# Optimization experiments

Hardware: AMD Instinct MI355X
Metric: run time of the kernel (lower is better)

## Reference

```python
import jax, jax.numpy as jnp
import numpy as np

B, S, D, V, H, L = 2, 64, 1024, 32000, 8, 2
HD = D // H

def setup_inputs():
    key = jax.random.key(0)
    ks = jax.random.split(key, 12)
    w = lambda k, shp: jax.random.normal(k, shp, jnp.float32) * 0.02
    return {
        "embedded_answer": jax.random.normal(ks[0], (B, S, D), jnp.float32),
        "sa_in_w": w(ks[1], (L, 3 * D, D)), "sa_in_b": jnp.zeros((L, 3 * D), jnp.float32),
        "sa_out_w": w(ks[2], (L, D, D)), "sa_out_b": jnp.zeros((L, D), jnp.float32),
        "ca_in_w": w(ks[3], (L, 3 * D, D)), "ca_in_b": jnp.zeros((L, 3 * D), jnp.float32),
        "ca_out_w": w(ks[4], (L, D, D)), "ca_out_b": jnp.zeros((L, D), jnp.float32),
        "ff1_w": w(ks[5], (L, 4 * D, D)), "ff1_b": jnp.zeros((L, 4 * D), jnp.float32),
        "ff2_w": w(ks[6], (L, D, 4 * D)), "ff2_b": jnp.zeros((L, D), jnp.float32),
        "ln_w": jnp.ones((L, 3, D), jnp.float32), "ln_b": jnp.zeros((L, 3, D), jnp.float32),
        "out_w": w(ks[7], (V, D)), "out_b": jnp.zeros((V,), jnp.float32),
        "temp_w": w(ks[8], (1, D)), "temp_b": jnp.zeros((1,), jnp.float32),
        "len_w": w(ks[9], (1, D)), "len_b": jnp.zeros((1,), jnp.float32),
        "style_w": w(ks[10], (D, D)), "style_b": jnp.zeros((D,), jnp.float32),
        "num_steps": 8,
    }

def _ln(x, w, b, eps=1e-5):
    m = x.mean(-1, keepdims=True)
    v = ((x - m) ** 2).mean(-1, keepdims=True)
    return (x - m) * jax.lax.rsqrt(v + eps) * w + b

def _mha(q_in, kv_in, in_w, in_b, ow, ob):
    wq, wk, wv = jnp.split(in_w, 3, 0)
    bq, bk, bv = jnp.split(in_b, 3, 0)
    q = (q_in @ wq.T + bq).reshape(q_in.shape[0], q_in.shape[1], H, HD)
    k = (kv_in @ wk.T + bk).reshape(kv_in.shape[0], kv_in.shape[1], H, HD)
    v = (kv_in @ wv.T + bv).reshape(kv_in.shape[0], kv_in.shape[1], H, HD)
    a = jax.nn.softmax(jnp.einsum('bqhd,bkhd->bhqk', q, k) * (HD ** -0.5), axis=-1)
    o = jnp.einsum('bhqk,bkhd->bqhd', a, v).reshape(q_in.shape)
    return o @ ow.T + ob

def _decode(x, mem, l, p):
    # post-LN torch TransformerDecoderLayer (relu FFN, no masks, eval/no dropout)
    x = _ln(x + _mha(x, x, p['sa_in_w'][l], p['sa_in_b'][l], p['sa_out_w'][l], p['sa_out_b'][l]), p['ln_w'][l, 0], p['ln_b'][l, 0])
    x = _ln(x + _mha(x, mem, p['ca_in_w'][l], p['ca_in_b'][l], p['ca_out_w'][l], p['ca_out_b'][l]), p['ln_w'][l, 1], p['ln_b'][l, 1])
    h = jax.nn.relu(x @ p['ff1_w'][l].T + p['ff1_b'][l]) @ p['ff2_w'][l].T + p['ff2_b'][l]
    return _ln(x + h, p['ln_w'][l, 2], p['ln_b'][l, 2])

def reference(embedded_answer, sa_in_w, sa_in_b, sa_out_w, sa_out_b, ca_in_w, ca_in_b, ca_out_w, ca_out_b, ff1_w, ff1_b, ff2_w, ff2_b, ln_w, ln_b, out_w, out_b, temp_w, temp_b, len_w, len_b, style_w, style_b, num_steps):
    p = dict(sa_in_w=sa_in_w, sa_in_b=sa_in_b, sa_out_w=sa_out_w, sa_out_b=sa_out_b,
             ca_in_w=ca_in_w, ca_in_b=ca_in_b, ca_out_w=ca_out_w, ca_out_b=ca_out_b,
             ff1_w=ff1_w, ff1_b=ff1_b, ff2_w=ff2_w, ff2_b=ff2_b, ln_w=ln_w, ln_b=ln_b)
    # control_generation (per-batch mean temperature / mean style vector)
    temp = jax.nn.sigmoid(embedded_answer @ temp_w.T + temp_b).mean(axis=(1, 2))[:, None]  # [B,1]
    _length_factor = jax.nn.sigmoid(embedded_answer @ len_w.T + len_b)  # drives static num_steps
    style = (embedded_answer @ style_w.T + style_b).mean(axis=1, keepdims=True)  # [B,1,D]
    cur = embedded_answer
    skey = jax.random.key(42)
    toks, lgs = [], []
    for t in range(num_steps):  # static unrolled decode loop; full recompute (no KV cache), as original
        h = cur
        for l in range(L):
            h = _decode(h, embedded_answer, l, p)
        logits_last = ((h + style)[:, -1, :] @ out_w.T + out_b) / temp  # [B,V]
        nt = jax.random.categorical(jax.random.fold_in(skey, t), logits_last)  # == softmax+multinomial
        toks.append(nt)
        lgs.append(logits_last)
        cur = jnp.concatenate([cur, out_w[nt][:, None, :]], axis=1)  # re-embed via output weight rows
    return jnp.stack(toks, 1), jnp.stack(lgs, 1)
```

## Files before the change

### kernel.cpp

```cpp
#include <hip/hip_runtime.h>
#include <stdint.h>

__host__ __device__ inline void threefry2x32(uint32_t k0, uint32_t k1,
                                             uint32_t x0, uint32_t x1,
                                             uint32_t* o0, uint32_t* o1) {
  uint32_t ks2 = 0x1BD11BDAu ^ k0 ^ k1;
  x0 += k0; x1 += k1;
#define TF_R(x, r) (((x) << (r)) | ((x) >> (32 - (r))))
#define TF_ROUND(r) { x0 += x1; x1 = TF_R(x1, r); x1 ^= x0; }
  TF_ROUND(13) TF_ROUND(15) TF_ROUND(26) TF_ROUND(6)
  x0 += k1; x1 += ks2 + 1u;
  TF_ROUND(17) TF_ROUND(29) TF_ROUND(16) TF_ROUND(24)
  x0 += ks2; x1 += k0 + 2u;
  TF_ROUND(13) TF_ROUND(15) TF_ROUND(26) TF_ROUND(6)
  x0 += k0; x1 += k1 + 3u;
  TF_ROUND(17) TF_ROUND(29) TF_ROUND(16) TF_ROUND(24)
  x0 += k1; x1 += ks2 + 4u;
  TF_ROUND(13) TF_ROUND(15) TF_ROUND(26) TF_ROUND(6)
  x0 += ks2; x1 += k0 + 5u;
  *o0 = x0; *o1 = x1;
#undef TF_ROUND
#undef TF_R
}

__device__ __forceinline__ float wave_sum(float v) {
#pragma unroll
  for (int o = 32; o > 0; o >>= 1) v += __shfl_xor(v, o, 64);
  return v;
}
__device__ __forceinline__ float wave_max(float v) {
#pragma unroll
  for (int o = 32; o > 0; o >>= 1) v = fmaxf(v, __shfl_xor(v, o, 64));
  return v;
}

__global__ __launch_bounds__(256) void gemm2_kernel(
    const float* __restrict__ X, long long xbs, int ldx,
    const float* __restrict__ W, int ldw,
    const float* __restrict__ bias,
    float* __restrict__ out, long long obs, int ldo,
    int St, int M, int N, int K32, int relu, int partial) {
  __shared__ __align__(16) float Xl[2][32][68];
  __shared__ __align__(16) float Wl[2][32][68];
  const int tid = threadIdx.x;
  const int m0 = blockIdx.x * 64;
  const int n0 = blockIdx.y * 64;
  const long long kbase = (long long)blockIdx.z * K32 * 32;
  const int mi = tid >> 4;
  const int ni = tid & 15;
  const int lr = tid >> 3;
  const int lc = (tid & 7) * 4;

  const int mA = m0 + lr, mB = m0 + lr + 32;
  const float* xpA = nullptr;
  const float* xpB = nullptr;
  if (mA < M) {
    int b = mA / St, s = mA - b * St;
    xpA = X + (long long)b * xbs + (long long)s * ldx + kbase + lc;
  }
  if (mB < M) {
    int b = mB / St, s = mB - b * St;
    xpB = X + (long long)b * xbs + (long long)s * ldx + kbase + lc;
  }
  const float* wpA = W + (long long)(n0 + lr) * ldw + kbase + lc;
  const float* wpB = W + (long long)(n0 + lr + 32) * ldw + kbase + lc;

  float4 xA = xpA ? *(const float4*)xpA : make_float4(0.f, 0.f, 0.f, 0.f);
  float4 xB = xpB ? *(const float4*)xpB : make_float4(0.f, 0.f, 0.f, 0.f);
  float4 wA = *(const float4*)wpA;
  float4 wB = *(const float4*)wpB;

  float acc[4][4];
#pragma unroll
  for (int i = 0; i < 4; ++i)
#pragma unroll
    for (int j = 0; j < 4; ++j) acc[i][j] = 0.f;

  Xl[0][lc + 0][lr] = xA.x; Xl[0][lc + 1][lr] = xA.y;
  Xl[0][lc + 2][lr] = xA.z; Xl[0][lc + 3][lr] = xA.w;
  Xl[0][lc + 0][lr + 32] = xB.x; Xl[0][lc + 1][lr + 32] = xB.y;
  Xl[0][lc + 2][lr + 32] = xB.z; Xl[0][lc + 3][lr + 32] = xB.w;
  Wl[0][lc + 0][lr] = wA.x; Wl[0][lc + 1][lr] = wA.y;
  Wl[0][lc + 2][lr] = wA.z; Wl[0][lc + 3][lr] = wA.w;
  Wl[0][lc + 0][lr + 32] = wB.x; Wl[0][lc + 1][lr + 32] = wB.y;
  Wl[0][lc + 2][lr + 32] = wB.z; Wl[0][lc + 3][lr + 32] = wB.w;
  __syncthreads();

  for (int i = 0; i < K32; ++i) {
    if (i + 1 < K32) {
      int off = (i + 1) * 32;
      xA = xpA ? *(const float4*)(xpA + off) : make_float4(0.f, 0.f, 0.f, 0.f);
      xB = xpB ? *(const float4*)(xpB + off) : make_float4(0.f, 0.f, 0.f, 0.f);
      wA = *(const float4*)(wpA + off);
      wB = *(const float4*)(wpB + off);
    }
    const int cur = i & 1;
#pragma unroll
    for (int kk = 0; kk < 32; ++kk) {
      float4 xv = *(const float4*)&Xl[cur][kk][mi * 4];
      float4 wv = *(const float4*)&Wl[cur][kk][ni * 4];
      float xa[4] = {xv.x, xv.y, xv.z, xv.w};
      float wa[4] = {wv.x, wv.y, wv.z, wv.w};
#pragma unroll
      for (int a = 0; a < 4; ++a)
#pragma unroll
        for (int c = 0; c < 4; ++c) acc[a][c] = fmaf(xa[a], wa[c], acc[a][c]);
    }
    if (i + 1 < K32) {
      __syncthreads();
      const int nxt = cur ^ 1;
      Xl[nxt][lc + 0][lr] = xA.x; Xl[nxt][lc + 1][lr] = xA.y;
      Xl[nxt][lc + 2][lr] = xA.z; Xl[nxt][lc + 3][lr] = xA.w;
      Xl[nxt][lc + 0][lr + 32] = xB.x; Xl[nxt][lc + 1][lr + 32] = xB.y;
      Xl[nxt][lc + 2][lr + 32] = xB.z; Xl[nxt][lc + 3][lr + 32] = xB.w;
      Wl[nxt][lc + 0][lr] = wA.x; Wl[nxt][lc + 1][lr] = wA.y;
      Wl[nxt][lc + 2][lr] = wA.z; Wl[nxt][lc + 3][lr] = wA.w;
      Wl[nxt][lc + 0][lr + 32] = wB.x; Wl[nxt][lc + 1][lr + 32] = wB.y;
      Wl[nxt][lc + 2][lr + 32] = wB.z; Wl[nxt][lc + 3][lr + 32] = wB.w;
      __syncthreads();
    }
  }

  const int n = n0 + ni * 4;
  if (partial) {
    float* base = out + (long long)blockIdx.z * M * ldo;
#pragma unroll
    for (int i = 0; i < 4; ++i) {
      int m = m0 + mi * 4 + i;
      if (m >= M) continue;
      *(float4*)(base + (long long)m * ldo + n) =
          make_float4(acc[i][0], acc[i][1], acc[i][2], acc[i][3]);
    }
  } else {
    float4 bv = *(const float4*)(bias + n);
#pragma unroll
    for (int i = 0; i < 4; ++i) {
      int m = m0 + mi * 4 + i;
      if (m >= M) continue;
      int b = m / St, s = m - b * St;
      float4 o;
      o.x = acc[i][0] + bv.x; o.y = acc[i][1] + bv.y;
      o.z = acc[i][2] + bv.z; o.w = acc[i][3] + bv.w;
      if (relu) {
        o.x = fmaxf(o.x, 0.f); o.y = fmaxf(o.y, 0.f);
        o.z = fmaxf(o.z, 0.f); o.w = fmaxf(o.w, 0.f);
      }
      *(float4*)(out + (long long)b * obs + (long long)s * ldo + n) = o;
    }
  }
}

__global__ __launch_bounds__(256) void epi_kernel(
    const float* __restrict__ P, int splits, int M, int N,
    const float* __restrict__ bias,
    const float* __restrict__ res, long long rbs, int ldr,
    const float* __restrict__ lnw, const float* __restrict__ lnb,
    float* __restrict__ out, long long obs, int ldo, int St, int relu) {
  __shared__ float red[4];
  const int m = blockIdx.x;
  const int b = m / St, s = m - b * St;
  const int n = blockIdx.y * 1024 + threadIdx.x * 4;
  const float* pr = P + (long long)m * N + n;
  float4 v = *(const float4*)pr;
  for (int sp = 1; sp < splits; ++sp) {
    float4 w2 = *(const float4*)(pr + (long long)sp * M * N);
    v.x += w2.x; v.y += w2.y; v.z += w2.z; v.w += w2.w;
  }
  float4 bv = *(const float4*)(bias + n);
  v.x += bv.x; v.y += bv.y; v.z += bv.z; v.w += bv.w;
  if (res) {
    float4 rv = *(const float4*)(res + (long long)b * rbs + (long long)s * ldr + n);
    v.x += rv.x; v.y += rv.y; v.z += rv.z; v.w += rv.w;
  }
  if (relu) {
    v.x = fmaxf(v.x, 0.f); v.y = fmaxf(v.y, 0.f);
    v.z = fmaxf(v.z, 0.f); v.w = fmaxf(v.w, 0.f);
  }
  if (lnw) {
    const int tid = threadIdx.x;
    float sum = wave_sum(v.x + v.y + v.z + v.w);
    int wid = tid >> 6;
    if ((tid & 63) == 0) red[wid] = sum;
    __syncthreads();
    float mean = (red[0] + red[1] + red[2] + red[3]) * (1.f / 1024.f);
    float4 d;
    d.x = v.x - mean; d.y = v.y - mean; d.z = v.z - mean; d.w = v.w - mean;
    float s2 = wave_sum(d.x * d.x + d.y * d.y + d.z * d.z + d.w * d.w);
    __syncthreads();
    if ((tid & 63) == 0) red[wid] = s2;
    __syncthreads();
    float var = (red[0] + red[1] + red[2] + red[3]) * (1.f / 1024.f);
    float inv = rsqrtf(var + 1e-5f);
    float4 wv = *(const float4*)(lnw + tid * 4);
    float4 lb = *(const float4*)(lnb + tid * 4);
    v.x = d.x * inv * wv.x + lb.x;
    v.y = d.y * inv * wv.y + lb.y;
    v.z = d.z * inv * wv.z + lb.z;
    v.w = d.w * inv * wv.w + lb.w;
  }
  *(float4*)(out + (long long)b * obs + (long long)s * ldo + n) = v;
}

__global__ __launch_bounds__(64) void attn_kernel(
    const float* __restrict__ Qp, int q_rs, long long q_bs,
    const float* __restrict__ Qp2,
    const float* __restrict__ qbias,
    const float* __restrict__ Kp, int k_rs, long long k_bs,
    const float* __restrict__ Vp, int v_rs, long long v_bs,
    float* __restrict__ Op, int o_rs, long long o_bs,
    int Sq, int Skv) {
  const int lane = threadIdx.x;
  int bid = blockIdx.x;
  int b = bid / (8 * Sq);
  int rr = bid - b * 8 * Sq;
  int h = rr / Sq;
  int sq = rr - h * Sq;
  const float* qrow = Qp + (long long)b * q_bs + (long long)sq * q_rs + h * 128;
  float q0 = qrow[lane], q1 = qrow[lane + 64];
  if (Qp2) {
    const float* q2 = Qp2 + (long long)b * q_bs + (long long)sq * q_rs + h * 128;
    q0 += q2[lane]; q1 += q2[lane + 64];
  }
  if (qbias) {
    q0 += qbias[h * 128 + lane]; q1 += qbias[h * 128 + lane + 64];
  }
  __shared__ float sc[72];
  const float* kb = Kp + (long long)b * k_bs + h * 128;
  for (int sk = 0; sk < Skv; ++sk) {
    const float* kr = kb + (long long)sk * k_rs;
    float p = fmaf(q0, kr[lane], q1 * kr[lane + 64]);
    p = wave_sum(p);
    if (lane == 0) sc[sk] = p * 0.08838834764831845f;
  }
  __syncthreads();
  float m = -3.4e38f;
  for (int i = lane; i < Skv; i += 64) m = fmaxf(m, sc[i]);
  m = wave_max(m);
  float ssum = 0.f;
  for (int i = lane; i < Skv; i += 64) {
    float e = expf(sc[i] - m);
    sc[i] = e;
    ssum += e;
  }
  ssum = wave_sum(ssum);
  __syncthreads();
  float o0 = 0.f, o1 = 0.f;
  const float* vb = Vp + (long long)b * v_bs + h * 128;
  for (int sk = 0; sk < Skv; ++sk) {
    float w = sc[sk];
    const float* vr = vb + (long long)sk * v_rs;
    o0 = fmaf(w, vr[lane], o0);
    o1 = fmaf(w, vr[lane + 64], o1);
  }
  float inv = 1.f / ssum;
  float* orow = Op + (long long)b * o_bs + (long long)sq * o_rs + h * 128;
  orow[lane] = o0 * inv;
  orow[lane + 64] = o1 * inv;
}

__global__ __launch_bounds__(256) void copy_cur_kernel(
    const float* __restrict__ emb, float* __restrict__ cur) {
  int idx = blockIdx.x * 256 + threadIdx.x;
  int b = idx >> 16;
  int r = idx & 65535;
  cur[(long long)b * 73728 + r] = emb[idx];
}

__global__ __launch_bounds__(256) void xmean_kernel(
    const float* __restrict__ emb, float* __restrict__ xmean) {
  int idx = blockIdx.x * 256 + threadIdx.x;
  int b = idx >> 10, d = idx & 1023;
  float s = 0.f;
  for (int ss = 0; ss < 64; ++ss) s += emb[b * 65536 + ss * 1024 + d];
  xmean[idx] = s * (1.f / 64.f);
}

__global__ __launch_bounds__(256) void temp_kernel(
    const float* __restrict__ emb, const float* __restrict__ tw,
    const float* __restrict__ tb, float* __restrict__ tempv) {
  __shared__ float red[4];
  int b = blockIdx.x;
  int wid = threadIdx.x >> 6, lane = threadIdx.x & 63;
  float acc = 0.f;
  for (int s = wid; s < 64; s += 4) {
    const float* x = emb + b * 65536 + s * 1024;
    float p = 0.f;
#pragma unroll
    for (int it = 0; it < 4; ++it) {
      float4 xv = *(const float4*)(x + it * 256 + lane * 4);
      float4 wv = *(const float4*)(tw + it * 256 + lane * 4);
      p += xv.x * wv.x + xv.y * wv.y + xv.z * wv.z + xv.w * wv.w;
    }
    p = wave_sum(p);
    acc += 1.f / (1.f + expf(-(p + tb[0])));
  }
  if (lane == 0) red[wid] = acc;
  __syncthreads();
  if (threadIdx.x == 0)
    tempv[b] = (red[0] + red[1] + red[2] + red[3]) * (1.f / 64.f);
}

__global__ __launch_bounds__(256) void style_kernel(
    const float* __restrict__ xmean, const float* __restrict__ sw,
    const float* __restrict__ sb, float* __restrict__ stylev) {
  int wid = threadIdx.x >> 6, lane = threadIdx.x & 63;
  int d = blockIdx.x * 4 + wid;
  const float* wr = sw + (long long)d * 1024;
  float a0 = 0.f, a1 = 0.f;
#pragma unroll
  for (int it = 0; it < 4; ++it) {
    float4 wv = *(const float4*)(wr + it * 256 + lane * 4);
    float4 x0 = *(const float4*)(xmean + it * 256 + lane * 4);
    float4 x1 = *(const float4*)(xmean + 1024 + it * 256 + lane * 4);
    a0 += wv.x * x0.x + wv.y * x0.y + wv.z * x0.z + wv.w * x0.w;
    a1 += wv.x * x1.x + wv.y * x1.y + wv.z * x1.z + wv.w * x1.w;
  }
  a0 = wave_sum(a0);
  a1 = wave_sum(a1);
  if (lane == 0) {
    stylev[d] = a0 + sb[d];
    stylev[1024 + d] = a1 + sb[d];
  }
}

__global__ __launch_bounds__(256) void logits_kernel(
    const float* __restrict__ A, const float* __restrict__ stylev, int St,
    const float* __restrict__ Wo, const float* __restrict__ bo,
    const float* __restrict__ tempv, float* __restrict__ outl, int t) {
  int wid = threadIdx.x >> 6, lane = threadIdx.x & 63;
  int n = blockIdx.x * 4 + wid;
  const float* wr = Wo + (long long)n * 1024;
  const float* a0p = A + (long long)(St - 1) * 1024;
  const float* a1p = A + 73728 + (long long)(St - 1) * 1024;
  float a0 = 0.f, a1 = 0.f;
#pragma unroll
  for (int it = 0; it < 4; ++it) {
    int off = it * 256 + lane * 4;
    float4 wv = *(const float4*)(wr + off);
    float4 x0 = *(const float4*)(a0p + off);
    float4 s0 = *(const float4*)(stylev + off);
    float4 x1 = *(const float4*)(a1p + off);
    float4 s1 = *(const float4*)(stylev + 1024 + off);
    float4 z0 = make_float4(x0.x + s0.x, x0.y + s0.y, x0.z + s0.z, x0.w + s0.w);
    float4 z1 = make_float4(x1.x + s1.x, x1.y + s1.y, x1.z + s1.z, x1.w + s1.w);
    a0 += wv.x * z0.x + wv.y * z0.y + wv.z * z0.z + wv.w * z0.w;
    a1 += wv.x * z1.x + wv.y * z1.y + wv.z * z1.z + wv.w * z1.w;
  }
  a0 = wave_sum(a0);
  a1 = wave_sum(a1);
  if (lane == 0) {
    float bb = bo[n];
    outl[(long long)(0 * 8 + t) * 32000 + n] = (a0 + bb) / tempv[0];
    outl[(long long)(1 * 8 + t) * 32000 + n] = (a1 + bb) / tempv[1];
  }
}

__global__ __launch_bounds__(1024) void sample_kernel(
    const float* __restrict__ logits, const float* __restrict__ Wo,
    float* __restrict__ tok_f, float* __restrict__ cur, int St,
    uint32_t fk0, uint32_t fk1, int t) {
  int b = blockIdx.x;
  const float* lg = logits + (long long)(b * 8 + t) * 32000;
  float best = -3.4e38f;
  int bi = 0x7fffffff;
  for (int n = threadIdx.x; n < 32000; n += 1024) {
    uint32_t r0, r1;
    threefry2x32(fk0, fk1, 0u, (uint32_t)(b * 32000 + n), &r0, &r1);
    uint32_t bits = (r0 ^ r1) >> 9;
    float u = __uint_as_float(0x3f800000u | bits) - 1.0f;
    if (u < 1.1754944e-38f) u = 1.1754944e-38f;
    float g = -logf(-logf(u));
    float val = lg[n] + g;
    if (val > best) { best = val; bi = n; }
  }
  __shared__ float bv[1024];
  __shared__ int bix[1024];
  bv[threadIdx.x] = best;
  bix[threadIdx.x] = bi;
  __syncthreads();
  for (int s = 512; s > 0; s >>= 1) {
    if (threadIdx.x < s) {
      float ov = bv[threadIdx.x + s];
      int oi = bix[threadIdx.x + s];
      if (ov > bv[threadIdx.x] ||
          (ov == bv[threadIdx.x] && oi < bix[threadIdx.x])) {
        bv[threadIdx.x] = ov;
        bix[threadIdx.x] = oi;
      }
    }
    __syncthreads();
  }
  int tok = bix[0];
  if (threadIdx.x == 0) tok_f[b * 8 + t] = (float)tok;
  cur[(long long)b * 73728 + (long long)St * 1024 + threadIdx.x] =
      Wo[(long long)tok * 1024 + threadIdx.x];
}

static inline void g2(hipStream_t st, const float* X, long long xbs, int ldx,
                      const float* W, int ldw, const float* bias, float* out,
                      long long obs, int ldo, int St, int M, int N, int K,
                      int splits, int relu, int partial) {
  dim3 grid((unsigned)((M + 63) / 64), (unsigned)(N / 64), (unsigned)splits);
  gemm2_kernel<<<grid, 256, 0, st>>>(X, xbs, ldx, W, ldw, bias, out, obs, ldo,
                                     St, M, N, K / (32 * splits), relu,
                                     partial);
}

static inline void epi(hipStream_t st, const float* P, int splits, int M,
                       int N, const float* bias, const float* res,
                       long long rbs, int ldr, const float* lnw,
                       const float* lnb, float* out, long long obs, int ldo,
                       int St, int relu) {
  dim3 grid((unsigned)M, (unsigned)(N / 1024));
  epi_kernel<<<grid, 256, 0, st>>>(P, splits, M, N, bias, res, rbs, ldr, lnw,
                                   lnb, out, obs, ldo, St, relu);
}

extern "C" void kernel_launch(void* const* d_in, const int* in_sizes, int n_in,
                              void* d_out, int out_size, void* d_ws,
                              size_t ws_size, hipStream_t stream) {
  const float* emb = (const float*)d_in[0];
  const float* sa_in_w = (const float*)d_in[1];
  const float* sa_in_b = (const float*)d_in[2];
  const float* sa_out_w = (const float*)d_in[3];
  const float* sa_out_b = (const float*)d_in[4];
  const float* ca_in_w = (const float*)d_in[5];
  const float* ca_in_b = (const float*)d_in[6];
  const float* ca_out_w = (const float*)d_in[7];
  const float* ca_out_b = (const float*)d_in[8];
  const float* ff1_w = (const float*)d_in[9];
  const float* ff1_b = (const float*)d_in[10];
  const float* ff2_w = (const float*)d_in[11];
  const float* ff2_b = (const float*)d_in[12];
  const float* ln_w = (const float*)d_in[13];
  const float* ln_b = (const float*)d_in[14];
  const float* out_w = (const float*)d_in[15];
  const float* out_b = (const float*)d_in[16];
  const float* temp_w = (const float*)d_in[17];
  const float* temp_b = (const float*)d_in[18];
  const float* style_w = (const float*)d_in[21];
  const float* style_b = (const float*)d_in[22];

  float* ws = (float*)d_ws;
  float* cur = ws;
  float* A = cur + 2 * 72 * 1024;
  float* Qb = A + 2 * 72 * 1024;
  float* Tb = Qb + 2 * 72 * 3072;
  float* Fb = Tb + 2 * 72 * 1024;
  float* cakv = Fb + 2 * 72 * 4096;
  float* Pp = cakv + 2 * 2 * 64 * 2048;
  float* xmean = Pp + 1310720;
  float* stylev = xmean + 2048;
  float* tempv = stylev + 2048;

  float* toks_out = (float*)d_out;
  float* logits_out = toks_out + 16;

  copy_cur_kernel<<<512, 256, 0, stream>>>(emb, cur);
  xmean_kernel<<<8, 256, 0, stream>>>(emb, xmean);
  temp_kernel<<<2, 256, 0, stream>>>(emb, temp_w, temp_b, tempv);
  style_kernel<<<256, 256, 0, stream>>>(xmean, style_w, style_b, stylev);
  for (int l = 0; l < 2; ++l) {
    g2(stream, emb, 64 * 1024, 1024,
       ca_in_w + (size_t)(l * 3072 + 1024) * 1024, 1024,
       ca_in_b + l * 3072 + 1024, cakv + (size_t)l * 2 * 64 * 2048, 64 * 2048,
       2048, 64, 128, 2048, 1024, 1, 0, 0);
  }

  for (int t = 0; t < 8; ++t) {
    int St = 64 + t;
    int M = 2 * St;
    for (int l = 0; l < 2; ++l) {
      const float* P0 = (l == 0) ? cur : A;
      g2(stream, P0, 72 * 1024, 1024, sa_in_w + (size_t)l * 3072 * 1024, 1024,
         sa_in_b + l * 3072, Qb, 72 * 3072, 3072, St, M, 3072, 1024, 1, 0, 0);
      attn_kernel<<<2 * 8 * St, 64, 0, stream>>>(
          Qb, 3072, 72 * 3072, nullptr, nullptr, Qb + 1024, 3072, 72 * 3072,
          Qb + 2048, 3072, 72 * 3072, Tb, 1024, 72 * 1024, St, St);
      g2(stream, Tb, 72 * 1024, 1024, sa_out_w + (size_t)l * 1024 * 1024, 1024,
         nullptr, Pp, 0, 1024, St, M, 1024, 1024, 4, 0, 1);
      epi(stream, Pp, 4, M, 1024, sa_out_b + l * 1024, P0, 72 * 1024, 1024,
          ln_w + (l * 3 + 0) * 1024, ln_b + (l * 3 + 0) * 1024, A, 72 * 1024,
          1024, St, 0);
      g2(stream, A, 72 * 1024, 1024, ca_in_w + (size_t)l * 3072 * 1024, 1024,
         nullptr, Pp, 0, 1024, St, M, 1024, 1024, 2, 0, 1);
      attn_kernel<<<2 * 8 * St, 64, 0, stream>>>(
          Pp, 1024, (long long)St * 1024, Pp + (size_t)M * 1024,
          ca_in_b + l * 3072, cakv + (size_t)l * 2 * 64 * 2048, 2048,
          64 * 2048, cakv + (size_t)l * 2 * 64 * 2048 + 1024, 2048, 64 * 2048,
          Tb, 1024, 72 * 1024, St, 64);
      g2(stream, Tb, 72 * 1024, 1024, ca_out_w + (size_t)l * 1024 * 1024, 1024,
         nullptr, Pp, 0, 1024, St, M, 1024, 1024, 4, 0, 1);
      epi(stream, Pp, 4, M, 1024, ca_out_b + l * 1024, A, 72 * 1024, 1024,
          ln_w + (l * 3 + 1) * 1024, ln_b + (l * 3 + 1) * 1024, A, 72 * 1024,
          1024, St, 0);
      g2(stream, A, 72 * 1024, 1024, ff1_w + (size_t)l * 4096 * 1024, 1024,
         ff1_b + l * 4096, Fb, 72 * 4096, 4096, St, M, 4096, 1024, 1, 1, 0);
      g2(stream, Fb, 72 * 4096, 4096, ff2_w + (size_t)l * 1024 * 4096, 4096,
         nullptr, Pp, 0, 1024, St, M, 1024, 4096, 8, 0, 1);
      epi(stream, Pp, 8, M, 1024, ff2_b + l * 1024, A, 72 * 1024, 1024,
          ln_w + (l * 3 + 2) * 1024, ln_b + (l * 3 + 2) * 1024, A, 72 * 1024,
          1024, St, 0);
    }
    logits_kernel<<<8000, 256, 0, stream>>>(A, stylev, St, out_w, out_b,
                                            tempv, logits_out, t);
    uint32_t fk0, fk1;
    threefry2x32(0u, 42u, 0u, (uint32_t)t, &fk0, &fk1);
    sample_kernel<<<2, 1024, 0, stream>>>(logits_out, out_w, toks_out, cur,
                                          St, fk0, fk1, t);
  }
}
```

Measured before the change: 5.834 ms.

## Fuse split-K reduction, residual and LayerNorm into GEMM via last-block atomics

Replaces the separate GEMM plus epilogue kernels with one GEMM that writes split-K partials and lets the last arriving block per tile, found with an atomic counter, reduce them and add bias, residual and ReLU. A second counter per row lets the last tile compute LayerNorm statistics. The normalization is then applied lazily when the next GEMM, the residual path or the logits kernel loads the data. Split counts go up for most GEMMs to raise parallelism. This removes the epilogue launches and their extra passes over memory, at the cost of threadfences, atomics, more partial-buffer traffic and recomputing the normalization on every load.

```diff
diff --git a/kernel.cpp b/kernel.cpp
--- a/kernel.cpp
+++ b/kernel.cpp
@@ -34,47 +34,73 @@
   return v;
 }
 
-__global__ __launch_bounds__(256) void gemm2_kernel(
+__global__ __launch_bounds__(256) void gemm3_kernel(
     const float* __restrict__ X, long long xbs, int ldx,
-    const float* __restrict__ W, int ldw,
-    const float* __restrict__ bias,
-    float* __restrict__ out, long long obs, int ldo,
-    int St, int M, int N, int K32, int relu, int partial) {
+    const float* __restrict__ xstats, const float* __restrict__ xlnw,
+    const float* __restrict__ xlnb,
+    const float* __restrict__ W, int ldw, const float* __restrict__ bias,
+    const float* __restrict__ resY, long long rbs, int ldr,
+    const float* __restrict__ rstats, const float* __restrict__ rlnw,
+    const float* __restrict__ rlnb,
+    float* __restrict__ Pp, float* __restrict__ out, long long obs, int ldo,
+    float* __restrict__ ostats,
+    int St, int M, int N, int K32, int relu,
+    int* __restrict__ tilecnt, int* __restrict__ rowcnt) {
   __shared__ __align__(16) float Xl[2][32][68];
   __shared__ __align__(16) float Wl[2][32][68];
+  __shared__ int sflag;
   const int tid = threadIdx.x;
   const int m0 = blockIdx.x * 64;
   const int n0 = blockIdx.y * 64;
+  const int splits = gridDim.z;
+  const int Nt = gridDim.y;
   const long long kbase = (long long)blockIdx.z * K32 * 32;
-  const int mi = tid >> 4;
-  const int ni = tid & 15;
-  const int lr = tid >> 3;
-  const int lc = (tid & 7) * 4;
+  const int mi = tid >> 4, ni = tid & 15, lr = tid >> 3, lc = (tid & 7) * 4;
+  const int wid = tid >> 6, lane = tid & 63;
 
   const int mA = m0 + lr, mB = m0 + lr + 32;
   const float* xpA = nullptr;
   const float* xpB = nullptr;
+  float mnA = 0.f, rsA = 1.f, mnB = 0.f, rsB = 1.f;
   if (mA < M) {
     int b = mA / St, s = mA - b * St;
     xpA = X + (long long)b * xbs + (long long)s * ldx + kbase + lc;
+    if (xstats) { mnA = xstats[2 * mA]; rsA = xstats[2 * mA + 1]; }
   }
   if (mB < M) {
     int b = mB / St, s = mB - b * St;
     xpB = X + (long long)b * xbs + (long long)s * ldx + kbase + lc;
+    if (xstats) { mnB = xstats[2 * mB]; rsB = xstats[2 * mB + 1]; }
   }
   const float* wpA = W + (long long)(n0 + lr) * ldw + kbase + lc;
   const float* wpB = W + (long long)(n0 + lr + 32) * ldw + kbase + lc;
+  const float* lwp = xlnw ? xlnw + kbase + lc : nullptr;
+  const float* lbp = xlnb ? xlnb + kbase + lc : nullptr;
 
   float4 xA = xpA ? *(const float4*)xpA : make_float4(0.f, 0.f, 0.f, 0.f);
   float4 xB = xpB ? *(const float4*)xpB : make_float4(0.f, 0.f, 0.f, 0.f);
   float4 wA = *(const float4*)wpA;
   float4 wB = *(const float4*)wpB;
+  float4 lw4 = make_float4(1.f, 1.f, 1.f, 1.f);
+  float4 lb4 = make_float4(0.f, 0.f, 0.f, 0.f);
+  if (lwp) { lw4 = *(const float4*)lwp; lb4 = *(const float4*)lbp; }
 
   float acc[4][4];
 #pragma unroll
   for (int i = 0; i < 4; ++i)
 #pragma unroll
     for (int j = 0; j < 4; ++j) acc[i][j] = 0.f;
+
+  if (xstats) {
+    xA.x = (xA.x - mnA) * rsA * lw4.x + lb4.x;
+    xA.y = (xA.y - mnA) * rsA * lw4.y + lb4.y;
+    xA.z = (xA.z - mnA) * rsA * lw4.z + lb4.z;
+    xA.w = (xA.w - mnA) * rsA * lw4.w + lb4.w;
+    xB.x = (xB.x - mnB) * rsB * lw4.x + lb4.x;
+    xB.y = (xB.y - mnB) * rsB * lw4.y + lb4.y;
+    xB.z = (xB.z - mnB) * rsB * lw4.z + lb4.z;
+    xB.w = (xB.w - mnB) * rsB * lw4.w + lb4.w;
+  }
 
   Xl[0][lc + 0][lr] = xA.x; Xl[0][lc + 1][lr] = xA.y;
   Xl[0][lc + 2][lr] = xA.z; Xl[0][lc + 3][lr] = xA.w;
@@ -93,6 +119,10 @@
       xB = xpB ? *(const float4*)(xpB + off) : make_float4(0.f, 0.f, 0.f, 0.f);
       wA = *(const float4*)(wpA + off);
       wB = *(const float4*)(wpB + off);
+      if (lwp) {
+        lw4 = *(const float4*)(lwp + off);
+        lb4 = *(const float4*)(lbp + off);
+      }
     }
     const int cur = i & 1;
 #pragma unroll
@@ -102,11 +132,22 @@
       float xa[4] = {xv.x, xv.y, xv.z, xv.w};
       float wa[4] = {wv.x, wv.y, wv.z, wv.w};
 #pragma unroll
-      for (int a = 0; a < 4; ++a)
-#pragma unroll
-        for (int c = 0; c < 4; ++c) acc[a][c] = fmaf(xa[a], wa[c], acc[a][c]);
+      for (int a2 = 0; a2 < 4; ++a2)
+#pragma unroll
+        for (int c2 = 0; c2 < 4; ++c2)
+          acc[a2][c2] = fmaf(xa[a2], wa[c2], acc[a2][c2]);
     }
     if (i + 1 < K32) {
+      if (xstats) {
+        xA.x = (xA.x - mnA) * rsA * lw4.x + lb4.x;
+        xA.y = (xA.y - mnA) * rsA * lw4.y + lb4.y;
+        xA.z = (xA.z - mnA) * rsA * lw4.z + lb4.z;
+        xA.w = (xA.w - mnA) * rsA * lw4.w + lb4.w;
+        xB.x = (xB.x - mnB) * rsB * lw4.x + lb4.x;
+        xB.y = (xB.y - mnB) * rsB * lw4.y + lb4.y;
+        xB.z = (xB.z - mnB) * rsB * lw4.z + lb4.z;
+        xB.w = (xB.w - mnB) * rsB * lw4.w + lb4.w;
+      }
       __syncthreads();
       const int nxt = cur ^ 1;
       Xl[nxt][lc + 0][lr] = xA.x; Xl[nxt][lc + 1][lr] = xA.y;
@@ -122,89 +163,97 @@
   }
 
   const int n = n0 + ni * 4;
-  if (partial) {
-    float* base = out + (long long)blockIdx.z * M * ldo;
+  {
+    float* base = Pp + (long long)blockIdx.z * M * N;
 #pragma unroll
     for (int i = 0; i < 4; ++i) {
       int m = m0 + mi * 4 + i;
       if (m >= M) continue;
-      *(float4*)(base + (long long)m * ldo + n) =
+      *(float4*)(base + (long long)m * N + n) =
           make_float4(acc[i][0], acc[i][1], acc[i][2], acc[i][3]);
     }
-  } else {
-    float4 bv = *(const float4*)(bias + n);
-#pragma unroll
-    for (int i = 0; i < 4; ++i) {
-      int m = m0 + mi * 4 + i;
+  }
+  __threadfence();
+  __syncthreads();
+  if (tid == 0)
+    sflag = (atomicAdd(tilecnt + blockIdx.y * gridDim.x + blockIdx.x, 1) ==
+             splits - 1);
+  __syncthreads();
+  if (!sflag) return;
+  __threadfence();
+
+  float4 bv = *(const float4*)(bias + n);
+#pragma unroll
+  for (int i = 0; i < 4; ++i) {
+    int m = m0 + mi * 4 + i;
+    if (m >= M) continue;
+    float4 v = make_float4(0.f, 0.f, 0.f, 0.f);
+    for (int sp = 0; sp < splits; ++sp) {
+      float4 p = *(const float4*)(Pp + (long long)sp * M * N +
+                                  (long long)m * N + n);
+      v.x += p.x; v.y += p.y; v.z += p.z; v.w += p.w;
+    }
+    v.x += bv.x; v.y += bv.y; v.z += bv.z; v.w += bv.w;
+    int b = m / St, s = m - b * St;
+    if (resY) {
+      float4 rv =
+          *(const float4*)(resY + (long long)b * rbs + (long long)s * ldr + n);
+      if (rstats) {
+        float rm = rstats[2 * m], rr = rstats[2 * m + 1];
+        float4 rw = *(const float4*)(rlnw + n);
+        float4 rb2 = *(const float4*)(rlnb + n);
+        rv.x = (rv.x - rm) * rr * rw.x + rb2.x;
+        rv.y = (rv.y - rm) * rr * rw.y + rb2.y;
+        rv.z = (rv.z - rm) * rr * rw.z + rb2.z;
+        rv.w = (rv.w - rm) * rr * rw.w + rb2.w;
+      }
+      v.x += rv.x; v.y += rv.y; v.z += rv.z; v.w += rv.w;
+    }
+    if (relu) {
+      v.x = fmaxf(v.x, 0.f); v.y = fmaxf(v.y, 0.f);
+      v.z = fmaxf(v.z, 0.f); v.w = fmaxf(v.w, 0.f);
+    }
+    *(float4*)(out + (long long)b * obs + (long long)s * ldo + n) = v;
+  }
+
+  if (ostats) {
+    __threadfence();
+    __syncthreads();
+    if (tid == 0)
+      sflag = (atomicAdd(rowcnt + blockIdx.x, 1) == Nt - 1);
+    __syncthreads();
+    if (!sflag) return;
+    __threadfence();
+    for (int r = wid; r < 64; r += 4) {
+      int m = m0 + r;
       if (m >= M) continue;
       int b = m / St, s = m - b * St;
-      float4 o;
-      o.x = acc[i][0] + bv.x; o.y = acc[i][1] + bv.y;
-      o.z = acc[i][2] + bv.z; o.w = acc[i][3] + bv.w;
-      if (relu) {
-        o.x = fmaxf(o.x, 0.f); o.y = fmaxf(o.y, 0.f);
-        o.z = fmaxf(o.z, 0.f); o.w = fmaxf(o.w, 0.f);
-      }
-      *(float4*)(out + (long long)b * obs + (long long)s * ldo + n) = o;
-    }
-  }
-}
-
-__global__ __launch_bounds__(256) void epi_kernel(
-    const float* __restrict__ P, int splits, int M, int N,
-    const float* __restrict__ bias,
-    const float* __restrict__ res, long long rbs, int ldr,
-    const float* __restrict__ lnw, const float* __restrict__ lnb,
-    float* __restrict__ out, long long obs, int ldo, int St, int relu) {
-  __shared__ float red[4];
-  const int m = blockIdx.x;
-  const int b = m / St, s = m - b * St;
-  const int n = blockIdx.y * 1024 + threadIdx.x * 4;
-  const float* pr = P + (long long)m * N + n;
-  float4 v = *(const float4*)pr;
-  for (int sp = 1; sp < splits; ++sp) {
-    float4 w2 = *(const float4*)(pr + (long long)sp * M * N);
-    v.x += w2.x; v.y += w2.y; v.z += w2.z; v.w += w2.w;
-  }
-  float4 bv = *(const float4*)(bias + n);
-  v.x += bv.x; v.y += bv.y; v.z += bv.z; v.w += bv.w;
-  if (res) {
-    float4 rv = *(const float4*)(res + (long long)b * rbs + (long long)s * ldr + n);
-    v.x += rv.x; v.y += rv.y; v.z += rv.z; v.w += rv.w;
-  }
-  if (relu) {
-    v.x = fmaxf(v.x, 0.f); v.y = fmaxf(v.y, 0.f);
-    v.z = fmaxf(v.z, 0.f); v.w = fmaxf(v.w, 0.f);
-  }
-  if (lnw) {
-    const int tid = threadIdx.x;
-    float sum = wave_sum(v.x + v.y + v.z + v.w);
-    int wid = tid >> 6;
-    if ((tid & 63) == 0) red[wid] = sum;
-    __syncthreads();
-    float mean = (red[0] + red[1] + red[2] + red[3]) * (1.f / 1024.f);
-    float4 d;
-    d.x = v.x - mean; d.y = v.y - mean; d.z = v.z - mean; d.w = v.w - mean;
-    float s2 = wave_sum(d.x * d.x + d.y * d.y + d.z * d.z + d.w * d.w);
-    __syncthreads();
-    if ((tid & 63) == 0) red[wid] = s2;
-    __syncthreads();
-    float var = (red[0] + red[1] + red[2] + red[3]) * (1.f / 1024.f);
-    float inv = rsqrtf(var + 1e-5f);
-    float4 wv = *(const float4*)(lnw + tid * 4);
-    float4 lb = *(const float4*)(lnb + tid * 4);
-    v.x = d.x * inv * wv.x + lb.x;
-    v.y = d.y * inv * wv.y + lb.y;
-    v.z = d.z * inv * wv.z + lb.z;
-    v.w = d.w * inv * wv.w + lb.w;
-  }
-  *(float4*)(out + (long long)b * obs + (long long)s * ldo + n) = v;
+      const float* row = out + (long long)b * obs + (long long)s * ldo;
+      float sm = 0.f;
+#pragma unroll
+      for (int it = 0; it < 4; ++it) {
+        float4 xv = *(const float4*)(row + it * 256 + lane * 4);
+        sm += xv.x + xv.y + xv.z + xv.w;
+      }
+      sm = wave_sum(sm) * (1.f / 1024.f);
+      float s2 = 0.f;
+#pragma unroll
+      for (int it = 0; it < 4; ++it) {
+        float4 xv = *(const float4*)(row + it * 256 + lane * 4);
+        float dx = xv.x - sm, dy = xv.y - sm, dz = xv.z - sm, dw = xv.w - sm;
+        s2 += dx * dx + dy * dy + dz * dz + dw * dw;
+      }
+      s2 = wave_sum(s2) * (1.f / 1024.f);
+      if (lane == 0) {
+        ostats[2 * m] = sm;
+        ostats[2 * m + 1] = rsqrtf(s2 + 1e-5f);
+      }
+    }
+  }
 }
 
 __global__ __launch_bounds__(64) void attn_kernel(
     const float* __restrict__ Qp, int q_rs, long long q_bs,
-    const float* __restrict__ Qp2,
-    const float* __restrict__ qbias,
     const float* __restrict__ Kp, int k_rs, long long k_bs,
     const float* __restrict__ Vp, int v_rs, long long v_bs,
     float* __restrict__ Op, int o_rs, long long o_bs,
@@ -217,13 +266,6 @@
   int sq = rr - h * Sq;
   const float* qrow = Qp + (long long)b * q_bs + (long long)sq * q_rs + h * 128;
   float q0 = qrow[lane], q1 = qrow[lane + 64];
-  if (Qp2) {
-    const float* q2 = Qp2 + (long long)b * q_bs + (long long)sq * q_rs + h * 128;
-    q0 += q2[lane]; q1 += q2[lane + 64];
-  }
-  if (qbias) {
-    q0 += qbias[h * 128 + lane]; q1 += qbias[h * 128 + lane + 64];
-  }
   __shared__ float sc[72];
   const float* kb = Kp + (long long)b * k_bs + h * 128;
   for (int sk = 0; sk < Skv; ++sk) {
@@ -324,27 +366,40 @@
 }
 
 __global__ __launch_bounds__(256) void logits_kernel(
-    const float* __restrict__ A, const float* __restrict__ stylev, int St,
-    const float* __restrict__ Wo, const float* __restrict__ bo,
-    const float* __restrict__ tempv, float* __restrict__ outl, int t) {
+    const float* __restrict__ Y, const float* __restrict__ ystats,
+    const float* __restrict__ lnw, const float* __restrict__ lnb, int St,
+    const float* __restrict__ stylev, const float* __restrict__ Wo,
+    const float* __restrict__ bo, const float* __restrict__ tempv,
+    float* __restrict__ outl, int t) {
   int wid = threadIdx.x >> 6, lane = threadIdx.x & 63;
   int n = blockIdx.x * 4 + wid;
   const float* wr = Wo + (long long)n * 1024;
-  const float* a0p = A + (long long)(St - 1) * 1024;
-  const float* a1p = A + 73728 + (long long)(St - 1) * 1024;
+  int m0 = St - 1, m1 = St + St - 1;
+  const float* y0 = Y + (long long)(St - 1) * 1024;
+  const float* y1 = Y + 73728 + (long long)(St - 1) * 1024;
+  float mean0 = ystats[2 * m0], rstd0 = ystats[2 * m0 + 1];
+  float mean1 = ystats[2 * m1], rstd1 = ystats[2 * m1 + 1];
   float a0 = 0.f, a1 = 0.f;
 #pragma unroll
   for (int it = 0; it < 4; ++it) {
     int off = it * 256 + lane * 4;
     float4 wv = *(const float4*)(wr + off);
-    float4 x0 = *(const float4*)(a0p + off);
+    float4 lw = *(const float4*)(lnw + off);
+    float4 lb = *(const float4*)(lnb + off);
     float4 s0 = *(const float4*)(stylev + off);
-    float4 x1 = *(const float4*)(a1p + off);
     float4 s1 = *(const float4*)(stylev + 1024 + off);
-    float4 z0 = make_float4(x0.x + s0.x, x0.y + s0.y, x0.z + s0.z, x0.w + s0.w);
-    float4 z1 = make_float4(x1.x + s1.x, x1.y + s1.y, x1.z + s1.z, x1.w + s1.w);
-    a0 += wv.x * z0.x + wv.y * z0.y + wv.z * z0.z + wv.w * z0.w;
-    a1 += wv.x * z1.x + wv.y * z1.y + wv.z * z1.z + wv.w * z1.w;
+    float4 x0 = *(const float4*)(y0 + off);
+    float4 x1 = *(const float4*)(y1 + off);
+    float z0x = (x0.x - mean0) * rstd0 * lw.x + lb.x + s0.x;
+    float z0y = (x0.y - mean0) * rstd0 * lw.y + lb.y + s0.y;
+    float z0z = (x0.z - mean0) * rstd0 * lw.z + lb.z + s0.z;
+    float z0w = (x0.w - mean0) * rstd0 * lw.w + lb.w + s0.w;
+    float z1x = (x1.x - mean1) * rstd1 * lw.x + lb.x + s1.x;
+    float z1y = (x1.y - mean1) * rstd1 * lw.y + lb.y + s1.y;
+    float z1z = (x1.z - mean1) * rstd1 * lw.z + lb.z + s1.z;
+    float z1w = (x1.w - mean1) * rstd1 * lw.w + lb.w + s1.w;
+    a0 += wv.x * z0x + wv.y * z0y + wv.z * z0z + wv.w * z0w;
+    a1 += wv.x * z1x + wv.y * z1y + wv.z * z1z + wv.w * z1w;
   }
   a0 = wave_sum(a0);
   a1 = wave_sum(a1);
@@ -394,26 +449,6 @@
   if (threadIdx.x == 0) tok_f[b * 8 + t] = (float)tok;
   cur[(long long)b * 73728 + (long long)St * 1024 + threadIdx.x] =
       Wo[(long long)tok * 1024 + threadIdx.x];
-}
-
-static inline void g2(hipStream_t st, const float* X, long long xbs, int ldx,
-                      const float* W, int ldw, const float* bias, float* out,
-                      long long obs, int ldo, int St, int M, int N, int K,
-                      int splits, int relu, int partial) {
-  dim3 grid((unsigned)((M + 63) / 64), (unsigned)(N / 64), (unsigned)splits);
-  gemm2_kernel<<<grid, 256, 0, st>>>(X, xbs, ldx, W, ldw, bias, out, obs, ldo,
-                                     St, M, N, K / (32 * splits), relu,
-                                     partial);
-}
-
-static inline void epi(hipStream_t st, const float* P, int splits, int M,
-                       int N, const float* bias, const float* res,
-                       long long rbs, int ldr, const float* lnw,
-                       const float* lnb, float* out, long long obs, int ldo,
-                       int St, int relu) {
-  dim3 grid((unsigned)M, (unsigned)(N / 1024));
-  epi_kernel<<<grid, 256, 0, st>>>(P, splits, M, N, bias, res, rbs, ldr, lnw,
-                                   lnb, out, obs, ldo, St, relu);
 }
 
 extern "C" void kernel_launch(void* const* d_in, const int* in_sizes, int n_in,
@@ -443,67 +478,102 @@
 
   float* ws = (float*)d_ws;
   float* cur = ws;
-  float* A = cur + 2 * 72 * 1024;
-  float* Qb = A + 2 * 72 * 1024;
-  float* Tb = Qb + 2 * 72 * 3072;
-  float* Fb = Tb + 2 * 72 * 1024;
-  float* cakv = Fb + 2 * 72 * 4096;
-  float* Pp = cakv + 2 * 2 * 64 * 2048;
-  float* xmean = Pp + 1310720;
+  float* Qb = cur + 147456;
+  float* Tb = Qb + 442368;
+  float* T2 = Tb + 147456;
+  float* Fb = T2 + 147456;
+  float* Yb = Fb + 589824;
+  float* cakv = Yb + 884736;
+  float* Pp = cakv + 524288;
+  float* xmean = Pp + 2400000;
   float* stylev = xmean + 2048;
   float* tempv = stylev + 2048;
+  float* statsb = tempv + 16;
+  int* cntpool = (int*)(statsb + 1728);
 
   float* toks_out = (float*)d_out;
   float* logits_out = toks_out + 16;
+
+  auto Y = [&](int l, int j) { return Yb + (size_t)(l * 3 + j) * 147456; };
+  auto SS = [&](int l, int j) { return statsb + (size_t)(l * 3 + j) * 288; };
+
+  hipMemsetAsync(cntpool, 0, 100 * 256 * sizeof(int), stream);
+
+  int inst = 0;
+  auto g3 = [&](const float* X, long long xbs, int ldx, const float* xst,
+                const float* xlw, const float* xlb, const float* W, int ldw,
+                const float* bias, const float* resY, long long rbs, int ldr,
+                const float* rst, const float* rlw, const float* rlb,
+                float* out, long long obs, int ldo, float* ost, int St, int M,
+                int N, int K, int splits, int relu) {
+    dim3 grid((unsigned)((M + 63) / 64), (unsigned)(N / 64),
+              (unsigned)splits);
+    int* tc = cntpool + inst * 256;
+    ++inst;
+    gemm3_kernel<<<grid, 256, 0, stream>>>(
+        X, xbs, ldx, xst, xlw, xlb, W, ldw, bias, resY, rbs, ldr, rst, rlw,
+        rlb, Pp, out, obs, ldo, ost, St, M, N, K / (32 * splits), relu, tc,
+        tc + 200);
+  };
 
   copy_cur_kernel<<<512, 256, 0, stream>>>(emb, cur);
   xmean_kernel<<<8, 256, 0, stream>>>(emb, xmean);
   temp_kernel<<<2, 256, 0, stream>>>(emb, temp_w, temp_b, tempv);
   style_kernel<<<256, 256, 0, stream>>>(xmean, style_w, style_b, stylev);
-  for (int l = 0; l < 2; ++l) {
-    g2(stream, emb, 64 * 1024, 1024,
+  for (int l = 0; l < 2; ++l)
+    g3(emb, 64 * 1024, 1024, nullptr, nullptr, nullptr,
        ca_in_w + (size_t)(l * 3072 + 1024) * 1024, 1024,
-       ca_in_b + l * 3072 + 1024, cakv + (size_t)l * 2 * 64 * 2048, 64 * 2048,
-       2048, 64, 128, 2048, 1024, 1, 0, 0);
-  }
+       ca_in_b + l * 3072 + 1024, nullptr, 0, 0, nullptr, nullptr, nullptr,
+       cakv + (size_t)l * 2 * 64 * 2048, 64 * 2048, 2048, nullptr, 64, 128,
+       2048, 1024, 4, 0);
 
   for (int t = 0; t < 8; ++t) {
-    int St = 64 + t;
-    int M = 2 * St;
+    const int St = 64 + t;
+    const int M = 2 * St;
     for (int l = 0; l < 2; ++l) {
-      const float* P0 = (l == 0) ? cur : A;
-      g2(stream, P0, 72 * 1024, 1024, sa_in_w + (size_t)l * 3072 * 1024, 1024,
-         sa_in_b + l * 3072, Qb, 72 * 3072, 3072, St, M, 3072, 1024, 1, 0, 0);
+      const float* X0 = (l == 0) ? cur : Y(0, 2);
+      const float* X0st = (l == 0) ? nullptr : SS(0, 2);
+      const float* X0lw = (l == 0) ? nullptr : ln_w + (0 * 3 + 2) * 1024;
+      const float* X0lb = (l == 0) ? nullptr : ln_b + (0 * 3 + 2) * 1024;
+
+      g3(X0, 72 * 1024, 1024, X0st, X0lw, X0lb,
+         sa_in_w + (size_t)l * 3072 * 1024, 1024, sa_in_b + l * 3072, nullptr,
+         0, 0, nullptr, nullptr, nullptr, Qb, 72 * 3072, 3072, nullptr, St, M,
+         3072, 1024, 4, 0);
       attn_kernel<<<2 * 8 * St, 64, 0, stream>>>(
-          Qb, 3072, 72 * 3072, nullptr, nullptr, Qb + 1024, 3072, 72 * 3072,
-          Qb + 2048, 3072, 72 * 3072, Tb, 1024, 72 * 1024, St, St);
-      g2(stream, Tb, 72 * 1024, 1024, sa_out_w + (size_t)l * 1024 * 1024, 1024,
-         nullptr, Pp, 0, 1024, St, M, 1024, 1024, 4, 0, 1);
-      epi(stream, Pp, 4, M, 1024, sa_out_b + l * 1024, P0, 72 * 1024, 1024,
-          ln_w + (l * 3 + 0) * 1024, ln_b + (l * 3 + 0) * 1024, A, 72 * 1024,
-          1024, St, 0);
-      g2(stream, A, 72 * 1024, 1024, ca_in_w + (size_t)l * 3072 * 1024, 1024,
-         nullptr, Pp, 0, 1024, St, M, 1024, 1024, 2, 0, 1);
+          Qb, 3072, 72 * 3072, Qb + 1024, 3072, 72 * 3072, Qb + 2048, 3072,
+          72 * 3072, Tb, 1024, 72 * 1024, St, St);
+      g3(Tb, 72 * 1024, 1024, nullptr, nullptr, nullptr,
+         sa_out_w + (size_t)l * 1024 * 1024, 1024, sa_out_b + l * 1024, X0,
+         72 * 1024, 1024, X0st, X0lw, X0lb, Y(l, 0), 72 * 1024, 1024,
+         SS(l, 0), St, M, 1024, 1024, 8, 0);
+      g3(Y(l, 0), 72 * 1024, 1024, SS(l, 0), ln_w + (l * 3 + 0) * 1024,
+         ln_b + (l * 3 + 0) * 1024, ca_in_w + (size_t)l * 3072 * 1024, 1024,
+         ca_in_b + l * 3072, nullptr, 0, 0, nullptr, nullptr, nullptr, T2,
+         72 * 1024, 1024, nullptr, St, M, 1024, 1024, 8, 0);
       attn_kernel<<<2 * 8 * St, 64, 0, stream>>>(
-          Pp, 1024, (long long)St * 1024, Pp + (size_t)M * 1024,
-          ca_in_b + l * 3072, cakv + (size_t)l * 2 * 64 * 2048, 2048,
+          T2, 1024, 72 * 1024, cakv + (size_t)l * 2 * 64 * 2048, 2048,
           64 * 2048, cakv + (size_t)l * 2 * 64 * 2048 + 1024, 2048, 64 * 2048,
           Tb, 1024, 72 * 1024, St, 64);
-      g2(stream, Tb, 72 * 1024, 1024, ca_out_w + (size_t)l * 1024 * 1024, 1024,
-         nullptr, Pp, 0, 1024, St, M, 1024, 1024, 4, 0, 1);
-      epi(stream, Pp, 4, M, 1024, ca_out_b + l * 1024, A, 72 * 1024, 1024,
-          ln_w + (l * 3 + 1) * 1024, ln_b + (l * 3 + 1) * 1024, A, 72 * 1024,
-          1024, St, 0);
-      g2(stream, A, 72 * 1024, 1024, ff1_w + (size_t)l * 4096 * 1024, 1024,
-         ff1_b + l * 4096, Fb, 72 * 4096, 4096, St, M, 4096, 1024, 1, 1, 0);
-      g2(stream, Fb, 72 * 4096, 4096, ff2_w + (size_t)l * 1024 * 4096, 4096,
-         nullptr, Pp, 0, 1024, St, M, 1024, 4096, 8, 0, 1);
-      epi(stream, Pp, 8, M, 1024, ff2_b + l * 1024, A, 72 * 1024, 1024,
-          ln_w + (l * 3 + 2) * 1024, ln_b + (l * 3 + 2) * 1024, A, 72 * 1024,
-          1024, St, 0);
-    }
-    logits_kernel<<<8000, 256, 0, stream>>>(A, stylev, St, out_w, out_b,
-                                            tempv, logits_out, t);
+      g3(Tb, 72 * 1024, 1024, nullptr, nullptr, nullptr,
+         ca_out_w + (size_t)l * 1024 * 1024, 1024, ca_out_b + l * 1024,
+         Y(l, 0), 72 * 1024, 1024, SS(l, 0), ln_w + (l * 3 + 0) * 1024,
+         ln_b + (l * 3 + 0) * 1024, Y(l, 1), 72 * 1024, 1024, SS(l, 1), St, M,
+         1024, 1024, 8, 0);
+      g3(Y(l, 1), 72 * 1024, 1024, SS(l, 1), ln_w + (l * 3 + 1) * 1024,
+         ln_b + (l * 3 + 1) * 1024, ff1_w + (size_t)l * 4096 * 1024, 1024,
+         ff1_b + l * 4096, nullptr, 0, 0, nullptr, nullptr, nullptr, Fb,
+         72 * 4096, 4096, nullptr, St, M, 4096, 1024, 4, 1);
+      g3(Fb, 72 * 4096, 4096, nullptr, nullptr, nullptr,
+         ff2_w + (size_t)l * 1024 * 4096, 4096, ff2_b + l * 1024, Y(l, 1),
+         72 * 1024, 1024, SS(l, 1), ln_w + (l * 3 + 1) * 1024,
+         ln_b + (l * 3 + 1) * 1024, Y(l, 2), 72 * 1024, 1024, SS(l, 2), St, M,
+         1024, 4096, 16, 0);
+    }
+    logits_kernel<<<8000, 256, 0, stream>>>(
+        Y(1, 2), SS(1, 2), ln_w + (1 * 3 + 2) * 1024,
+        ln_b + (1 * 3 + 2) * 1024, St, stylev, out_w, out_b, tempv,
+        logits_out, t);
     uint32_t fk0, fk1;
     threefry2x32(0u, 42u, 0u, (uint32_t)t, &fk0, &fk1);
     sample_kernel<<<2, 1024, 0, stream>>>(logits_out, out_w, toks_out, cur,
```

New measurement: 11.14 ms. 1.91x slower.
